# Kernel tuning notes

Measured on AMD Instinct MI355X. Metric: run time of the kernel, lower is better.

Reference implementation:

```python
import jax, jax.numpy as jnp
import numpy as np

BN_EPS = 1e-5


def _bn(x_proj, gamma, beta):
    # x_proj: [T, B, 3H]; BatchNorm1d(training) stats over (T, B) per channel.
    mean = jnp.mean(x_proj, axis=(0, 1))
    var = jnp.var(x_proj, axis=(0, 1))  # biased, as torch uses for normalization
    return (x_proj - mean) * (gamma / jnp.sqrt(var + BN_EPS)) + beta


def _gru_scan(x_proj, Wh, H):
    # x_proj: [T, B, 3H]; Wh: [3H, H] (torch Linear weight -> y = h @ Wh.T)
    B = x_proj.shape[1]
    h0 = jnp.zeros((B, H), dtype=x_proj.dtype)

    def step(h, xp):
        hp = h @ Wh.T  # [B, 3H]
        r = jax.nn.sigmoid(xp[:, :H] + hp[:, :H])
        z = jax.nn.sigmoid(xp[:, H:2 * H] + hp[:, H:2 * H])
        n = jnp.tanh(xp[:, 2 * H:] + r * hp[:, 2 * H:])
        h = (1.0 - z) * h + z * n
        return h, h

    _, hs = jax.lax.scan(step, h0, x_proj)
    return hs  # [T, B, H]


def setup_inputs() -> dict:
    key = jax.random.key(0)
    ks = jax.random.split(key, 4)
    T, B, D, H = 1024, 32, 512, 512
    x = jax.random.normal(ks[0], (T, B, D), dtype=jnp.float32)
    s = 0.05
    Wx = jax.random.normal(ks[1], (3 * H, D), dtype=jnp.float32) * s
    Wh_fwd = jax.random.normal(ks[2], (3 * H, H), dtype=jnp.float32) * s
    Wh_bwd = jax.random.normal(ks[3], (3 * H, H), dtype=jnp.float32) * s
    gamma = jnp.ones((3 * H,), dtype=jnp.float32)
    beta = jnp.zeros((3 * H,), dtype=jnp.float32)
    return {"x": x, "Wx": Wx, "Wh_fwd": Wh_fwd, "Wh_bwd": Wh_bwd,
            "gamma": gamma, "beta": beta}


def reference(x, Wx, Wh_fwd, Wh_bwd, gamma, beta):
    H = Wh_fwd.shape[1]
    x_proj = _bn(jnp.einsum('tbd,gd->tbg', x, Wx), gamma, beta)  # [T,B,3H]
    hs_fwd = _gru_scan(x_proj, Wh_fwd, H)
    hs_bwd = _gru_scan(x_proj[::-1], Wh_bwd, H)[::-1]
    return hs_fwd + hs_bwd
```

## Files before the change

### kernel.cpp

```cpp
#include <hip/hip_runtime.h>
#include <stdint.h>

#define T_LEN 1024
#define BATCH 32
#define DIN   512
#define HID   512
#define G3    1536
#define ROWS  (T_LEN*BATCH)
#define NSL   8
#define FSTR  16

typedef short bf16x8 __attribute__((ext_vector_type(8)));
typedef float f32x4  __attribute__((ext_vector_type(4)));
typedef uint32_t u32x4 __attribute__((ext_vector_type(4)));

__device__ __forceinline__ unsigned short f2bf(float f) {
  union { float f; uint32_t u; } v; v.f = f;
  uint32_t u = v.u;
  return (unsigned short)((u + 0x7fffu + ((u >> 16) & 1u)) >> 16);
}
__device__ __forceinline__ float bf2f(unsigned short h) {
  union { uint32_t u; float f; } v; v.u = ((uint32_t)h) << 16; return v.f;
}
__device__ __forceinline__ float sigm(float x)   { return 1.f / (1.f + __expf(-x)); }
__device__ __forceinline__ float tanh_f(float x) { return 2.f / (1.f + __expf(-2.f * x)) - 1.f; }

__global__ void zero_init(float* stats, int* flags) {
  int i = blockIdx.x * 256 + threadIdx.x;
  flags[i] = 0;
  if (i < 2 * G3) stats[i] = 0.f;
}

__global__ void convert_bf16(const float* __restrict__ src, unsigned short* __restrict__ dst, int n4) {
  int i = blockIdx.x * 256 + threadIdx.x;
  if (i < n4) {
    float4 v = ((const float4*)src)[i];
    ushort4 o;
    o.x = f2bf(v.x); o.y = f2bf(v.y); o.z = f2bf(v.z); o.w = f2bf(v.w);
    ((ushort4*)dst)[i] = o;
  }
}

__global__ __launch_bounds__(256) void gemm_proj(const unsigned short* __restrict__ xb,
                                                 const unsigned short* __restrict__ wxb,
                                                 unsigned short* __restrict__ P) {
  int w = threadIdx.x >> 6;
  int l = threadIdx.x & 63;
  int mi = w >> 1, ni = w & 1;
  int row_base = blockIdx.x * 64 + mi * 32;
  int col_base = blockIdx.y * 64 + ni * 32;
  int lr = l & 15, lk8 = (l >> 4) * 8;
  f32x4 acc00 = {0,0,0,0}, acc01 = {0,0,0,0}, acc10 = {0,0,0,0}, acc11 = {0,0,0,0};
  #pragma unroll 4
  for (int kk = 0; kk < 16; ++kk) {
    int k0 = kk * 32 + lk8;
    bf16x8 a0 = *(const bf16x8*)(xb  + (size_t)(row_base + lr) * DIN + k0);
    bf16x8 a1 = *(const bf16x8*)(xb  + (size_t)(row_base + 16 + lr) * DIN + k0);
    bf16x8 b0 = *(const bf16x8*)(wxb + (size_t)(col_base + lr) * DIN + k0);
    bf16x8 b1 = *(const bf16x8*)(wxb + (size_t)(col_base + 16 + lr) * DIN + k0);
    acc00 = __builtin_amdgcn_mfma_f32_16x16x32_bf16(a0, b0, acc00, 0, 0, 0);
    acc01 = __builtin_amdgcn_mfma_f32_16x16x32_bf16(a0, b1, acc01, 0, 0, 0);
    acc10 = __builtin_amdgcn_mfma_f32_16x16x32_bf16(a1, b0, acc10, 0, 0, 0);
    acc11 = __builtin_amdgcn_mfma_f32_16x16x32_bf16(a1, b1, acc11, 0, 0, 0);
  }
  int rrow = (l >> 4) * 4;
  #pragma unroll
  for (int r = 0; r < 4; ++r) {
    P[(size_t)(row_base +      rrow + r) * G3 + col_base +      lr] = f2bf(acc00[r]);
    P[(size_t)(row_base +      rrow + r) * G3 + col_base + 16 + lr] = f2bf(acc01[r]);
    P[(size_t)(row_base + 16 + rrow + r) * G3 + col_base +      lr] = f2bf(acc10[r]);
    P[(size_t)(row_base + 16 + rrow + r) * G3 + col_base + 16 + lr] = f2bf(acc11[r]);
  }
}

__global__ void bn_stats(const unsigned short* __restrict__ P, float* __restrict__ stats) {
  int col = blockIdx.x * 256 + threadIdx.x;
  int r0  = blockIdx.y * 512;
  float s = 0.f, q = 0.f;
  for (int r = 0; r < 512; ++r) {
    float v = bf2f(P[(size_t)(r0 + r) * G3 + col]);
    s += v; q += v * v;
  }
  atomicAdd(&stats[col], s);
  atomicAdd(&stats[G3 + col], q);
}

__global__ void bn_final(const float* __restrict__ stats, const float* __restrict__ gamma,
                         const float* __restrict__ beta, float* __restrict__ params) {
  int c = blockIdx.x * 256 + threadIdx.x;
  if (c >= G3) return;
  float mean = stats[c] * (1.f / ROWS);
  float var  = stats[G3 + c] * (1.f / ROWS) - mean * mean;
  float sc = gamma[c] * rsqrtf(var + 1e-5f);
  params[c] = sc;
  params[G3 + c] = beta[c] - mean * sc;
}

__global__ __launch_bounds__(256, 1) void scan_kernel(
    const unsigned short* __restrict__ P, const float* __restrict__ params,
    const unsigned short* __restrict__ whf, const unsigned short* __restrict__ whb,
    unsigned short* __restrict__ histf, unsigned short* __restrict__ histb,
    int* __restrict__ flags) {
  int blk = blockIdx.x;
  int d = blk >> 3;
  int s = blk & 7;
  int j0 = s * 64;
  int tid = threadIdx.x;
  int w = tid >> 6, l = tid & 63;
  int lr = l & 15, lk8 = (l >> 4) * 8;

  const unsigned short* wh = d ? whb : whf;
  unsigned short* myhist = d ? histb : histf;
  int* myflags = flags + (size_t)d * T_LEN * NSL * FSTR;

  bf16x8 bfrag[3][16];
  #pragma unroll
  for (int q = 0; q < 3; ++q) {
    int i = w * 3 + q;
    int cb = (i >> 2) * HID + j0 + (i & 3) * 16;
    const unsigned short* wrow = wh + (size_t)(cb + lr) * HID;
    #pragma unroll
    for (int kk = 0; kk < 16; ++kk)
      bfrag[q][kk] = *(const bf16x8*)(wrow + kk * 32 + lk8);
  }

  __shared__ __align__(16) char hlds[BATCH * HID * 2];
  __shared__ float hp[3][BATCH][66];

  int jp = tid & 31;
  int jc0 = j0 + jp * 2;
  float scr[2], shr[2], scz[2], shz[2], scn[2], shn[2];
  #pragma unroll
  for (int u = 0; u < 2; ++u) {
    int c = jc0 + u;
    scr[u] = params[c];           shr[u] = params[G3 + c];
    scz[u] = params[HID + c];     shz[u] = params[G3 + HID + c];
    scn[u] = params[2 * HID + c]; shn[u] = params[G3 + 2 * HID + c];
  }

  for (int t = 0; t < T_LEN; ++t) {
    int time = d ? (T_LEN - 1 - t) : t;

    uint32_t pr[4], pz[4], pn[4];
    #pragma unroll
    for (int i = 0; i < 4; ++i) {
      int b = (tid >> 5) + i * 8;
      const unsigned short* prow = P + (size_t)(time * BATCH + b) * G3 + jc0;
      pr[i] = *(const uint32_t*)(prow);
      pz[i] = *(const uint32_t*)(prow + HID);
      pn[i] = *(const uint32_t*)(prow + 2 * HID);
    }

    if (t > 0) {
      if (tid < NSL) {
        const int* fa = myflags + (size_t)(t - 1) * NSL * FSTR + tid * FSTR;
        int guard = 0, fv = 0;
        do {
          asm volatile("global_load_dword %0, %1, off sc0 sc1\n\ts_waitcnt vmcnt(0)"
                       : "=v"(fv) : "v"(fa) : "memory");
          if (++guard > (1 << 17)) break;
        } while (fv == 0);
      }
      __syncthreads();
      const char* hprev = (const char*)(myhist + (size_t)(t - 1) * BATCH * HID);
      u32x4 hv[8];
      #pragma unroll
      for (int i = 0; i < 8; ++i) {
        const char* a = hprev + (tid + i * 256) * 16;
        asm volatile("global_load_dwordx4 %0, %1, off sc0 sc1" : "=v"(hv[i]) : "v"(a));
      }
      asm volatile("s_waitcnt vmcnt(0)" ::: "memory");
      __builtin_amdgcn_sched_barrier(0);
      #pragma unroll
      for (int i = 0; i < 8; ++i) {
        int c = tid + i * 256;
        int row = c >> 6;
        *(u32x4*)(hlds + ((c * 16) ^ ((row & 7) << 4))) = hv[i];
      }
    } else {
      u32x4 z = {0, 0, 0, 0};
      #pragma unroll
      for (int i = 0; i < 8; ++i) {
        int c = tid + i * 256;
        *(u32x4*)(hlds + c * 16) = z;
      }
    }
    __syncthreads();

    f32x4 acc[2][3] = {};
    #pragma unroll
    for (int kk = 0; kk < 16; ++kk) {
      int cbase = kk * 64 + lk8 * 2;
      int sw = (lr & 7) << 4;
      bf16x8 a0 = *(const bf16x8*)(hlds + ((lr * 1024 + cbase) ^ sw));
      bf16x8 a1 = *(const bf16x8*)(hlds + (((lr + 16) * 1024 + cbase) ^ sw));
      #pragma unroll
      for (int q = 0; q < 3; ++q) {
        acc[0][q] = __builtin_amdgcn_mfma_f32_16x16x32_bf16(a0, bfrag[q][kk], acc[0][q], 0, 0, 0);
        acc[1][q] = __builtin_amdgcn_mfma_f32_16x16x32_bf16(a1, bfrag[q][kk], acc[1][q], 0, 0, 0);
      }
    }
    #pragma unroll
    for (int q = 0; q < 3; ++q) {
      int i = w * 3 + q;
      int g = i >> 2, ncol = (i & 3) * 16 + lr;
      #pragma unroll
      for (int m = 0; m < 2; ++m) {
        int rrow = m * 16 + (l >> 4) * 4;
        #pragma unroll
        for (int r = 0; r < 4; ++r) hp[g][rrow + r][ncol] = acc[m][q][r];
      }
    }
    __syncthreads();

    unsigned short* hout = myhist + (size_t)t * BATCH * HID;
    #pragma unroll
    for (int i = 0; i < 4; ++i) {
      int b = (tid >> 5) + i * 8;
      float2 rp2 = *(const float2*)&hp[0][b][2 * jp];
      float2 zp2 = *(const float2*)&hp[1][b][2 * jp];
      float2 np2 = *(const float2*)&hp[2][b][2 * jp];
      uint32_t hpair = *(const uint32_t*)(hlds + ((b * 1024 + jc0 * 2) ^ ((b & 7) << 4)));
      uint32_t o = 0;
      #pragma unroll
      for (int u = 0; u < 2; ++u) {
        float xrv = bf2f((unsigned short)((u ? (pr[i] >> 16) : pr[i]) & 0xffff));
        float xzv = bf2f((unsigned short)((u ? (pz[i] >> 16) : pz[i]) & 0xffff));
        float xnv = bf2f((unsigned short)((u ? (pn[i] >> 16) : pn[i]) & 0xffff));
        float rpv = u ? rp2.y : rp2.x;
        float zpv = u ? zp2.y : zp2.x;
        float npv = u ? np2.y : np2.x;
        float rv = sigm(fmaf(xrv, scr[u], shr[u]) + rpv);
        float zv = sigm(fmaf(xzv, scz[u], shz[u]) + zpv);
        float nv = tanh_f(fmaf(xnv, scn[u], shn[u]) + rv * npv);
        float hold = bf2f((unsigned short)((u ? (hpair >> 16) : hpair) & 0xffff));
        unsigned short ho = f2bf((1.f - zv) * hold + zv * nv);
        o |= ((uint32_t)ho) << (16 * u);
      }
      char* addr = (char*)(hout + (size_t)b * HID + jc0);
      asm volatile("global_store_dword %0, %1, off sc0 sc1" :: "v"(addr), "v"(o) : "memory");
    }
    asm volatile("s_waitcnt vmcnt(0)" ::: "memory");
    __syncthreads();
    if (tid == 0) {
      int* fa = myflags + (size_t)t * NSL * FSTR + s * FSTR;
      int one = 1;
      asm volatile("global_store_dword %0, %1, off sc0 sc1" :: "v"(fa), "v"(one) : "memory");
    }
  }
}

__global__ void final_add(const unsigned short* __restrict__ histf,
                          const unsigned short* __restrict__ histb,
                          float* __restrict__ out) {
  size_t i4 = (size_t)blockIdx.x * 256 + threadIdx.x;
  size_t e = i4 * 4;
  int t = (int)(e / (BATCH * HID));
  size_t rem = e % (BATCH * HID);
  ushort4 vf = *(const ushort4*)(histf + e);
  ushort4 vb = *(const ushort4*)(histb + (size_t)(T_LEN - 1 - t) * BATCH * HID + rem);
  float4 o;
  o.x = bf2f(vf.x) + bf2f(vb.x);
  o.y = bf2f(vf.y) + bf2f(vb.y);
  o.z = bf2f(vf.z) + bf2f(vb.z);
  o.w = bf2f(vf.w) + bf2f(vb.w);
  *(float4*)(out + e) = o;
}

extern "C" void kernel_launch(void* const* d_in, const int* in_sizes, int n_in,
                              void* d_out, int out_size, void* d_ws, size_t ws_size,
                              hipStream_t stream) {
  const float* x     = (const float*)d_in[0];
  const float* Wx    = (const float*)d_in[1];
  const float* Whf   = (const float*)d_in[2];
  const float* Whb   = (const float*)d_in[3];
  const float* gamma = (const float*)d_in[4];
  const float* beta  = (const float*)d_in[5];
  float* out = (float*)d_out;

  char* ws = (char*)d_ws;
  size_t off = 0;
  auto alloc = [&](size_t bytes) {
    char* p = ws + off;
    off += (bytes + 255) & ~(size_t)255;
    return p;
  };
  unsigned short* xb    = (unsigned short*)alloc((size_t)ROWS * DIN * 2);
  unsigned short* wxb   = (unsigned short*)alloc((size_t)G3 * DIN * 2);
  unsigned short* whfb  = (unsigned short*)alloc((size_t)G3 * HID * 2);
  unsigned short* whbb  = (unsigned short*)alloc((size_t)G3 * HID * 2);
  unsigned short* P     = (unsigned short*)alloc((size_t)ROWS * G3 * 2);
  float* stats          = (float*)alloc(2 * G3 * 4);
  float* params         = (float*)alloc(2 * G3 * 4);
  unsigned short* histf = (unsigned short*)alloc((size_t)T_LEN * BATCH * HID * 2);
  unsigned short* histb = (unsigned short*)alloc((size_t)T_LEN * BATCH * HID * 2);
  int* flags            = (int*)alloc((size_t)2 * T_LEN * NSL * FSTR * 4);

  hipLaunchKernelGGL(zero_init, dim3(1024), dim3(256), 0, stream, stats, flags);
  hipLaunchKernelGGL(convert_bf16, dim3(16384), dim3(256), 0, stream, x, xb, ROWS * DIN / 4);
  hipLaunchKernelGGL(convert_bf16, dim3(768), dim3(256), 0, stream, Wx, wxb, G3 * DIN / 4);
  hipLaunchKernelGGL(convert_bf16, dim3(768), dim3(256), 0, stream, Whf, whfb, G3 * HID / 4);
  hipLaunchKernelGGL(convert_bf16, dim3(768), dim3(256), 0, stream, Whb, whbb, G3 * HID / 4);
  hipLaunchKernelGGL(gemm_proj, dim3(512, 24), dim3(256), 0, stream, xb, wxb, P);
  hipLaunchKernelGGL(bn_stats, dim3(6, 64), dim3(256), 0, stream, P, stats);
  hipLaunchKernelGGL(bn_final, dim3(6), dim3(256), 0, stream, stats, gamma, beta, params);
  hipLaunchKernelGGL(scan_kernel, dim3(16), dim3(256), 0, stream,
                     P, params, whfb, whbb, histf, histb, flags);
  hipLaunchKernelGGL(final_add, dim3(16384), dim3(256), 0, stream, histf, histb, out);
}
```

Measured before the change: 5.670 ms.

## Replace per-step flag handshake with tagged mailbox carrying hidden state

The scan no longer publishes a per-slice flag after a store drain and barrier. Each bf16 hidden value is now written into a 4-deep ring mailbox as a 32-bit word whose upper half holds the step tag. Consumers poll the mailbox directly and retry only the chunks whose tags do not match yet. This removes the flag round trip and the vmcnt drain on the critical path of every timestep. In exchange it doubles the bytes exchanged per step, adds per-thread polling traffic, and assumes the mailbox never holds stale tags that match, since it is not zeroed between calls.

```diff
diff --git a/kernel.cpp b/kernel.cpp
--- a/kernel.cpp
+++ b/kernel.cpp
@@ -8,11 +8,12 @@
 #define G3    1536
 #define ROWS  (T_LEN*BATCH)
 #define NSL   8
-#define FSTR  16
+#define MBOX_DEPTH 4
 
 typedef short bf16x8 __attribute__((ext_vector_type(8)));
 typedef float f32x4  __attribute__((ext_vector_type(4)));
 typedef uint32_t u32x4 __attribute__((ext_vector_type(4)));
+typedef uint32_t u32x2 __attribute__((ext_vector_type(2)));
 
 __device__ __forceinline__ unsigned short f2bf(float f) {
   union { float f; uint32_t u; } v; v.f = f;
@@ -25,9 +26,8 @@
 __device__ __forceinline__ float sigm(float x)   { return 1.f / (1.f + __expf(-x)); }
 __device__ __forceinline__ float tanh_f(float x) { return 2.f / (1.f + __expf(-2.f * x)) - 1.f; }
 
-__global__ void zero_init(float* stats, int* flags) {
+__global__ void zero_init(float* stats) {
   int i = blockIdx.x * 256 + threadIdx.x;
-  flags[i] = 0;
   if (i < 2 * G3) stats[i] = 0.f;
 }
 
@@ -100,7 +100,7 @@
     const unsigned short* __restrict__ P, const float* __restrict__ params,
     const unsigned short* __restrict__ whf, const unsigned short* __restrict__ whb,
     unsigned short* __restrict__ histf, unsigned short* __restrict__ histb,
-    int* __restrict__ flags) {
+    uint32_t* __restrict__ mboxf, uint32_t* __restrict__ mboxb) {
   int blk = blockIdx.x;
   int d = blk >> 3;
   int s = blk & 7;
@@ -111,7 +111,7 @@
 
   const unsigned short* wh = d ? whb : whf;
   unsigned short* myhist = d ? histb : histf;
-  int* myflags = flags + (size_t)d * T_LEN * NSL * FSTR;
+  uint32_t* mybox = d ? mboxb : mboxf;
 
   bf16x8 bfrag[3][16];
   #pragma unroll
@@ -152,37 +152,49 @@
     }
 
     if (t > 0) {
-      if (tid < NSL) {
-        const int* fa = myflags + (size_t)(t - 1) * NSL * FSTR + tid * FSTR;
-        int guard = 0, fv = 0;
-        do {
-          asm volatile("global_load_dword %0, %1, off sc0 sc1\n\ts_waitcnt vmcnt(0)"
-                       : "=v"(fv) : "v"(fa) : "memory");
-          if (++guard > (1 << 17)) break;
-        } while (fv == 0);
-      }
-      __syncthreads();
-      const char* hprev = (const char*)(myhist + (size_t)(t - 1) * BATCH * HID);
-      u32x4 hv[8];
+      uint32_t expect = ((uint32_t)t) << 16;
+      const uint32_t* mb = mybox + (size_t)((t - 1) & (MBOX_DEPTH - 1)) * (BATCH * HID);
+      u32x4 hv[16];
+      uint32_t pend = 0xffffu;
+      int guard = 0;
+      do {
+        #pragma unroll
+        for (int i = 0; i < 16; ++i) {
+          if (pend & (1u << i)) {
+            const uint32_t* a = mb + (size_t)(tid + i * 256) * 4;
+            asm volatile("global_load_dwordx4 %0, %1, off sc0 sc1"
+                         : "=v"(hv[i]) : "v"(a) : "memory");
+          }
+        }
+        asm volatile("s_waitcnt vmcnt(0)" ::: "memory");
+        __builtin_amdgcn_sched_barrier(0);
+        #pragma unroll
+        for (int i = 0; i < 16; ++i) {
+          if (pend & (1u << i)) {
+            uint32_t diff = ((hv[i].x ^ expect) | (hv[i].y ^ expect) |
+                             (hv[i].z ^ expect) | (hv[i].w ^ expect)) & 0xffff0000u;
+            if (diff == 0) {
+              int c = tid + i * 256;
+              int row = c >> 7;
+              int colb = (c & 127) * 8;
+              u32x2 pk;
+              pk.x = (hv[i].x & 0xffffu) | (hv[i].y << 16);
+              pk.y = (hv[i].z & 0xffffu) | (hv[i].w << 16);
+              *(u32x2*)(hlds + ((row * 1024 + colb) ^ ((row & 7) << 4))) = pk;
+              pend &= ~(1u << i);
+            }
+          }
+        }
+        if (pend) { if (++guard > (1 << 13)) break; }
+      } while (pend);
+    } else {
+      u32x2 z = {0, 0};
       #pragma unroll
-      for (int i = 0; i < 8; ++i) {
-        const char* a = hprev + (tid + i * 256) * 16;
-        asm volatile("global_load_dwordx4 %0, %1, off sc0 sc1" : "=v"(hv[i]) : "v"(a));
-      }
-      asm volatile("s_waitcnt vmcnt(0)" ::: "memory");
-      __builtin_amdgcn_sched_barrier(0);
-      #pragma unroll
-      for (int i = 0; i < 8; ++i) {
+      for (int i = 0; i < 16; ++i) {
         int c = tid + i * 256;
-        int row = c >> 6;
-        *(u32x4*)(hlds + ((c * 16) ^ ((row & 7) << 4))) = hv[i];
-      }
-    } else {
-      u32x4 z = {0, 0, 0, 0};
-      #pragma unroll
-      for (int i = 0; i < 8; ++i) {
-        int c = tid + i * 256;
-        *(u32x4*)(hlds + c * 16) = z;
+        int row = c >> 7;
+        int colb = (c & 127) * 8;
+        *(u32x2*)(hlds + ((row * 1024 + colb) ^ ((row & 7) << 4))) = z;
       }
     }
     __syncthreads();
@@ -214,6 +226,8 @@
     __syncthreads();
 
     unsigned short* hout = myhist + (size_t)t * BATCH * HID;
+    uint32_t* mslot = mybox + (size_t)(t & (MBOX_DEPTH - 1)) * (BATCH * HID);
+    uint32_t tagw = ((uint32_t)(t + 1)) << 16;
     #pragma unroll
     for (int i = 0; i < 4; ++i) {
       int b = (tid >> 5) + i * 8;
@@ -237,16 +251,15 @@
         unsigned short ho = f2bf((1.f - zv) * hold + zv * nv);
         o |= ((uint32_t)ho) << (16 * u);
       }
-      char* addr = (char*)(hout + (size_t)b * HID + jc0);
-      asm volatile("global_store_dword %0, %1, off sc0 sc1" :: "v"(addr), "v"(o) : "memory");
-    }
-    asm volatile("s_waitcnt vmcnt(0)" ::: "memory");
+      *(uint32_t*)(hout + (size_t)b * HID + jc0) = o;
+      u32x2 tv;
+      tv.x = tagw | (o & 0xffffu);
+      tv.y = tagw | (o >> 16);
+      uint32_t* maddr = mslot + (size_t)b * HID + jc0;
+      asm volatile("global_store_dwordx2 %0, %1, off sc0 sc1"
+                   :: "v"(maddr), "v"(tv) : "memory");
+    }
     __syncthreads();
-    if (tid == 0) {
-      int* fa = myflags + (size_t)t * NSL * FSTR + s * FSTR;
-      int one = 1;
-      asm volatile("global_store_dword %0, %1, off sc0 sc1" :: "v"(fa), "v"(one) : "memory");
-    }
   }
 }
 
@@ -294,9 +307,10 @@
   float* params         = (float*)alloc(2 * G3 * 4);
   unsigned short* histf = (unsigned short*)alloc((size_t)T_LEN * BATCH * HID * 2);
   unsigned short* histb = (unsigned short*)alloc((size_t)T_LEN * BATCH * HID * 2);
-  int* flags            = (int*)alloc((size_t)2 * T_LEN * NSL * FSTR * 4);
-
-  hipLaunchKernelGGL(zero_init, dim3(1024), dim3(256), 0, stream, stats, flags);
+  uint32_t* mboxf       = (uint32_t*)alloc((size_t)MBOX_DEPTH * BATCH * HID * 4);
+  uint32_t* mboxb       = (uint32_t*)alloc((size_t)MBOX_DEPTH * BATCH * HID * 4);
+
+  hipLaunchKernelGGL(zero_init, dim3(12), dim3(256), 0, stream, stats);
   hipLaunchKernelGGL(convert_bf16, dim3(16384), dim3(256), 0, stream, x, xb, ROWS * DIN / 4);
   hipLaunchKernelGGL(convert_bf16, dim3(768), dim3(256), 0, stream, Wx, wxb, G3 * DIN / 4);
   hipLaunchKernelGGL(convert_bf16, dim3(768), dim3(256), 0, stream, Whf, whfb, G3 * HID / 4);
@@ -305,6 +319,6 @@
   hipLaunchKernelGGL(bn_stats, dim3(6, 64), dim3(256), 0, stream, P, stats);
   hipLaunchKernelGGL(bn_final, dim3(6), dim3(256), 0, stream, stats, gamma, beta, params);
   hipLaunchKernelGGL(scan_kernel, dim3(16), dim3(256), 0, stream,
-                     P, params, whfb, whbb, histf, histb, flags);
+                     P, params, whfb, whbb, histf, histb, mboxf, mboxb);
   hipLaunchKernelGGL(final_add, dim3(16384), dim3(256), 0, stream, histf, histb, out);
 }
```

After: 6.477 ms. +14.2%, slower.
